# Optimization experiments

Hardware: AMD Instinct MI355X
Metric: run time of the kernel (lower is better)

The kernel has to match this reference:

```python
import jax, jax.numpy as jnp
import numpy as np

B, S, P, J = 32, 128, 2, 17
DIN, DOUT, DRNN, DHID = 2, 3, 128, 256
N = P * J
DT = 0.1   # delta_t from init
K = 4      # Euler steps, hardcoded k=int(4) in source


def setup_inputs() -> dict:
    key = jax.random.key(0)
    ks = jax.random.split(key, 12)
    g = lambda k, sh, fan: (jax.random.normal(k, sh, jnp.float32) / np.sqrt(fan)).astype(jnp.float32)
    d = {}
    d['x2d'] = jax.random.normal(ks[0], (B, S, P, J, DIN), jnp.float32)
    d['mask'] = jax.random.randint(ks[1], (B, S, P, J, 1), 0, 2).astype(jnp.int32)
    # ODE MLP: DRNN -> DHID -> DHID -> DRNN (num_hidden=2 hidden layers, tanh)
    d['ode_w0'] = g(ks[2], (DRNN, DHID), DRNN); d['ode_b0'] = jnp.zeros((DHID,), jnp.float32)
    d['ode_w1'] = g(ks[3], (DHID, DHID), DHID); d['ode_b1'] = jnp.zeros((DHID,), jnp.float32)
    d['ode_w2'] = g(ks[4], (DHID, DRNN), DHID); d['ode_b2'] = jnp.zeros((DRNN,), jnp.float32)
    # GRU cell 0: input DIN -> hidden DRNN ; GRU cell 1: input DRNN -> hidden DRNN
    d['wih0'] = g(ks[5], (DIN, 3 * DRNN), DIN);  d['whh0'] = g(ks[6], (DRNN, 3 * DRNN), DRNN)
    d['bih0'] = jnp.zeros((3 * DRNN,), jnp.float32); d['bhh0'] = jnp.zeros((3 * DRNN,), jnp.float32)
    d['wih1'] = g(ks[7], (DRNN, 3 * DRNN), DRNN); d['whh1'] = g(ks[8], (DRNN, 3 * DRNN), DRNN)
    d['bih1'] = jnp.zeros((3 * DRNN,), jnp.float32); d['bhh1'] = jnp.zeros((3 * DRNN,), jnp.float32)
    d['wout'] = g(ks[9], (DRNN, DOUT), DRNN); d['bout'] = jnp.zeros((DOUT,), jnp.float32)
    d['h0'] = 0.01 * jax.random.normal(ks[10], (1, 1, DRNN), jnp.float32)
    return d


def _ode(h, w0, b0, w1, b1, w2, b2):
    h = jnp.tanh(h @ w0 + b0)
    h = jnp.tanh(h @ w1 + b1)
    return h @ w2 + b2


def _gru(x, h, wih, whh, bih, bhh):
    gi = x @ wih + bih
    gh = h @ whh + bhh
    ir, iz, ig = jnp.split(gi, 3, axis=-1)
    hr, hz, hg = jnp.split(gh, 3, axis=-1)
    r = jax.nn.sigmoid(ir + hr)
    z = jax.nn.sigmoid(iz + hz)
    n = jnp.tanh(ig + r * hg)
    return (1.0 - z) * n + z * h


def reference(x2d, mask, ode_w0, ode_b0, ode_w1, ode_b1, ode_w2, ode_b2,
              wih0, whh0, bih0, bhh0, wih1, whh1, bih1, bhh1, wout, bout, h0):
    m = mask.astype(x2d.dtype)                      # (B,S,P,J,1)
    xs = (x2d * m).reshape(B, S, N, DIN)            # masked 2D input
    ms = m.reshape(B, S, N, 1)
    h_init = jnp.broadcast_to(h0, (B, N, DRNN))

    def step(h, inp):
        x, mm = inp                                 # (B,N,DIN), (B,N,1)
        h1 = h
        for _ in range(K):                          # 4 Euler ODE steps
            h1 = h1 + DT * _ode(h1, ode_w0, ode_b0, ode_w1, ode_b1, ode_w2, ode_b2)
        h2 = _gru(x, h1, wih0, whh0, bih0, bhh0)    # stacked GRU, both conditioned on h1
        h2 = _gru(h2, h1, wih1, whh1, bih1, bhh1)
        h_next = h1 * (1.0 - mm) + h2 * mm
        return h_next, h1

    _, hs = jax.lax.scan(step, h_init,
                         (jnp.swapaxes(xs, 0, 1), jnp.swapaxes(ms, 0, 1)))
    hs = jnp.swapaxes(hs, 0, 1)                     # (B,S,N,DRNN)
    ys = (hs @ wout + bout).reshape(B, S, P, J, DOUT)
    return ys
```

## Files before the change

kernel.cpp:

```cpp
#include <hip/hip_runtime.h>

typedef _Float16 f16x8 __attribute__((ext_vector_type(8)));
typedef float f32x4 __attribute__((ext_vector_type(4)));

constexpr int S_ = 128;
constexpr float DT_ = 0.1f;
constexpr float LS = 2048.0f;
constexpr float INV = 1.0f / 2048.0f;

#define MFMA(a, b, c) __builtin_amdgcn_mfma_f32_16x16x32_f16((a), (b), (c), 0, 0, 0)

#define OB0   0
#define OB1   256
#define OB2   512
#define OBHH0 640
#define OBIH0 1024
#define OBIH1 1408
#define OBHH1 1792
#define NBIAS 2176

__device__ __forceinline__ float fast_tanh(float x) {
    float e = __expf(2.0f * x);
    return 1.0f - 2.0f / (e + 1.0f);
}
__device__ __forceinline__ float fast_sigmoid(float x) {
    return 1.0f / (1.0f + __expf(-x));
}

__global__ void prep_hl(const float* __restrict__ src, _Float16* __restrict__ hi,
                        _Float16* __restrict__ lo, int K, int N) {
    int e = blockIdx.x * 256 + threadIdx.x;
    if (e >= K * N) return;
    int tile = e >> 9, r = e & 511;
    int lane = r >> 3, j = r & 7;
    int KT = K >> 5;
    int nt = tile / KT, kt = tile - nt * KT;
    int k = kt * 32 + ((lane >> 4) << 3) + j;
    int n = nt * 16 + (lane & 15);
    float v = src[k * N + n];
    _Float16 h = (_Float16)v;
    hi[e] = h;
    lo[e] = (_Float16)((v - (float)h) * LS);
}

__global__ __launch_bounds__(512, 2) void odernn_mfma(
    const float* __restrict__ x2d, const int* __restrict__ maskp,
    const _Float16* __restrict__ w0h, const _Float16* __restrict__ w0l,
    const _Float16* __restrict__ w1hg, const _Float16* __restrict__ w1lg,
    const _Float16* __restrict__ w2h, const _Float16* __restrict__ w2l,
    const _Float16* __restrict__ hh0h, const _Float16* __restrict__ hh0l,
    const _Float16* __restrict__ ih1h, const _Float16* __restrict__ ih1l,
    const _Float16* __restrict__ hh1h, const _Float16* __restrict__ hh1l,
    const float* __restrict__ b0, const float* __restrict__ b1,
    const float* __restrict__ b2, const float* __restrict__ bhh0,
    const float* __restrict__ bih0, const float* __restrict__ wih0,
    const float* __restrict__ bih1, const float* __restrict__ bhh1,
    const float* __restrict__ wout, const float* __restrict__ bout,
    const float* __restrict__ h0, float* __restrict__ out)
{
    __shared__ float hF[16][128];
    __shared__ _Float16 bAh[16][264], bAl[16][264];
    __shared__ _Float16 bBh[16][264], bBl[16][264];
    __shared__ _Float16 bHh[16][136], bHl[16][136];
    __shared__ float sbias[NBIAS];
    __shared__ float swi0[768];
    __shared__ float swout[384];
    __shared__ float sbout[4];
    __shared__ float sx0[16], sx1[16], smm[16];
    __shared__ int sIdx[16];

    const int tid = (int)threadIdx.x;
    const int wv = tid >> 6;
    const int l = tid & 63;
    const int lrow = l & 15;
    const int lk8 = (l >> 4) << 3;
    const int rbase = (l >> 4) << 2;

    for (int e = tid; e < 256; e += 512) { sbias[OB0 + e] = b0[e]; sbias[OB1 + e] = b1[e]; }
    for (int e = tid; e < 128; e += 512) sbias[OB2 + e] = b2[e];
    for (int e = tid; e < 384; e += 512) {
        sbias[OBHH0 + e] = bhh0[e];
        sbias[OBIH0 + e] = bih0[e];
        sbias[OBIH1 + e] = bih1[e];
        sbias[OBHH1 + e] = bhh1[e];
        swout[e] = wout[e];
    }
    for (int e = tid; e < 768; e += 512) swi0[e] = wih0[e];
    if (tid < 3) sbout[tid] = bout[tid];
    for (int e = tid; e < 2048; e += 512) hF[e >> 7][e & 127] = h0[e & 127];
    if (tid < 16) {
        int grow = (int)blockIdx.x * 16 + tid;
        int bb = grow / 34, nn = grow - bb * 34;
        sIdx[tid] = bb * (S_ * 34) + nn;
    }

    f16x8 w1rh[2][8], w1rl[2][8];
#pragma unroll
    for (int t = 0; t < 2; ++t) {
        const _Float16* ph = w1hg + (size_t)((wv + 8 * t) * 8) * 512 + l * 8;
        const _Float16* pl = w1lg + (size_t)((wv + 8 * t) * 8) * 512 + l * 8;
#pragma unroll
        for (int kt = 0; kt < 8; ++kt) {
            w1rh[t][kt] = *(const f16x8*)(ph + kt * 512);
            w1rl[t][kt] = *(const f16x8*)(pl + kt * 512);
        }
    }
    __syncthreads();

    for (int s = 0; s < S_; ++s) {
        if (tid < 16) {
            int idx = sIdx[tid] + s * 34;
            float fm = (float)maskp[idx];
            smm[tid] = fm;
            sx0[tid] = x2d[2 * idx] * fm;
            sx1[tid] = x2d[2 * idx + 1] * fm;
        }
        for (int e = tid; e < 2048; e += 512) {
            int row = e >> 7, col = e & 127;
            float v = hF[row][col];
            _Float16 hh = (_Float16)v;
            bHh[row][col] = hh;
            bHl[row][col] = (_Float16)((v - (float)hh) * LS);
        }
        __syncthreads();

        for (int it = 0; it < 4; ++it) {
            {
                const int n0 = wv << 4, n1 = (wv + 8) << 4;
                float bv0 = sbias[OB0 + n0 + lrow], bv1 = sbias[OB0 + n1 + lrow];
                f32x4 a0 = {bv0, bv0, bv0, bv0}, a1 = {bv1, bv1, bv1, bv1};
                f32x4 e0 = {0, 0, 0, 0}, e1 = {0, 0, 0, 0};
                const f16x8* B0h = (const f16x8*)(w0h + (size_t)(wv * 4) * 512) + l;
                const f16x8* B0l = (const f16x8*)(w0l + (size_t)(wv * 4) * 512) + l;
                const f16x8* B1h = (const f16x8*)(w0h + (size_t)((wv + 8) * 4) * 512) + l;
                const f16x8* B1l = (const f16x8*)(w0l + (size_t)((wv + 8) * 4) * 512) + l;
#pragma unroll
                for (int kt = 0; kt < 4; ++kt) {
                    f16x8 ah = *(const f16x8*)&bHh[lrow][kt * 32 + lk8];
                    f16x8 al = *(const f16x8*)&bHl[lrow][kt * 32 + lk8];
                    f16x8 bh0 = B0h[kt * 64], bl0 = B0l[kt * 64];
                    f16x8 bh1 = B1h[kt * 64], bl1 = B1l[kt * 64];
                    a0 = MFMA(ah, bh0, a0);
                    e0 = MFMA(ah, bl0, e0);
                    e0 = MFMA(al, bh0, e0);
                    a1 = MFMA(ah, bh1, a1);
                    e1 = MFMA(ah, bl1, e1);
                    e1 = MFMA(al, bh1, e1);
                }
#pragma unroll
                for (int r = 0; r < 4; ++r) {
                    int row = rbase + r;
                    float v0 = fast_tanh(a0[r] + e0[r] * INV);
                    float v1 = fast_tanh(a1[r] + e1[r] * INV);
                    _Float16 hh = (_Float16)v0;
                    bBh[row][n0 + lrow] = hh;
                    bBl[row][n0 + lrow] = (_Float16)((v0 - (float)hh) * LS);
                    hh = (_Float16)v1;
                    bBh[row][n1 + lrow] = hh;
                    bBl[row][n1 + lrow] = (_Float16)((v1 - (float)hh) * LS);
                }
            }
            __syncthreads();

            {
                const int n0 = wv << 4, n1 = (wv + 8) << 4;
                float bv0 = sbias[OB1 + n0 + lrow], bv1 = sbias[OB1 + n1 + lrow];
                f32x4 a0 = {bv0, bv0, bv0, bv0}, a1 = {bv1, bv1, bv1, bv1};
                f32x4 e0 = {0, 0, 0, 0}, e1 = {0, 0, 0, 0};
#pragma unroll
                for (int kt = 0; kt < 8; ++kt) {
                    f16x8 ah = *(const f16x8*)&bBh[lrow][kt * 32 + lk8];
                    f16x8 al = *(const f16x8*)&bBl[lrow][kt * 32 + lk8];
                    a0 = MFMA(ah, w1rh[0][kt], a0);
                    e0 = MFMA(ah, w1rl[0][kt], e0);
                    e0 = MFMA(al, w1rh[0][kt], e0);
                    a1 = MFMA(ah, w1rh[1][kt], a1);
                    e1 = MFMA(ah, w1rl[1][kt], e1);
                    e1 = MFMA(al, w1rh[1][kt], e1);
                }
#pragma unroll
                for (int r = 0; r < 4; ++r) {
                    int row = rbase + r;
                    float v0 = fast_tanh(a0[r] + e0[r] * INV);
                    float v1 = fast_tanh(a1[r] + e1[r] * INV);
                    _Float16 hh = (_Float16)v0;
                    bAh[row][n0 + lrow] = hh;
                    bAl[row][n0 + lrow] = (_Float16)((v0 - (float)hh) * LS);
                    hh = (_Float16)v1;
                    bAh[row][n1 + lrow] = hh;
                    bAl[row][n1 + lrow] = (_Float16)((v1 - (float)hh) * LS);
                }
            }
            __syncthreads();

            {
                const int n0 = wv << 4;
                float bv = sbias[OB2 + n0 + lrow];
                f32x4 acc = {bv, bv, bv, bv};
                f32x4 ecc = {0, 0, 0, 0};
                const f16x8* Bh = (const f16x8*)(w2h + (size_t)(wv * 8) * 512) + l;
                const f16x8* Bl = (const f16x8*)(w2l + (size_t)(wv * 8) * 512) + l;
#pragma unroll
                for (int kt = 0; kt < 8; ++kt) {
                    f16x8 ah = *(const f16x8*)&bAh[lrow][kt * 32 + lk8];
                    f16x8 al = *(const f16x8*)&bAl[lrow][kt * 32 + lk8];
                    f16x8 bh = Bh[kt * 64], bl = Bl[kt * 64];
                    acc = MFMA(ah, bh, acc);
                    ecc = MFMA(ah, bl, ecc);
                    ecc = MFMA(al, bh, ecc);
                }
#pragma unroll
                for (int r = 0; r < 4; ++r) {
                    int row = rbase + r, col = n0 + lrow;
                    float v = hF[row][col] + DT_ * (acc[r] + ecc[r] * INV);
                    hF[row][col] = v;
                    _Float16 hh = (_Float16)v;
                    bHh[row][col] = hh;
                    bHl[row][col] = (_Float16)((v - (float)hh) * LS);
                }
            }
            __syncthreads();
        }

        {
            f32x4 acc0, acc1, acc2, ecc0, ecc1, ecc2;
            {
                float v0 = sbias[OBHH0 + ((wv) << 4) + lrow];
                float v1 = sbias[OBHH0 + ((wv + 8) << 4) + lrow];
                float v2 = sbias[OBHH0 + ((wv + 16) << 4) + lrow];
                acc0 = (f32x4){v0, v0, v0, v0};
                acc1 = (f32x4){v1, v1, v1, v1};
                acc2 = (f32x4){v2, v2, v2, v2};
                ecc0 = (f32x4){0, 0, 0, 0}; ecc1 = ecc0; ecc2 = ecc0;
            }
#pragma unroll
            for (int kt = 0; kt < 4; ++kt) {
                f16x8 ah = *(const f16x8*)&bHh[lrow][kt * 32 + lk8];
                f16x8 al = *(const f16x8*)&bHl[lrow][kt * 32 + lk8];
                f16x8 bh0 = *((const f16x8*)(hh0h + (size_t)((wv) * 4 + kt) * 512) + l);
                f16x8 bl0 = *((const f16x8*)(hh0l + (size_t)((wv) * 4 + kt) * 512) + l);
                f16x8 bh1 = *((const f16x8*)(hh0h + (size_t)((wv + 8) * 4 + kt) * 512) + l);
                f16x8 bl1 = *((const f16x8*)(hh0l + (size_t)((wv + 8) * 4 + kt) * 512) + l);
                f16x8 bh2 = *((const f16x8*)(hh0h + (size_t)((wv + 16) * 4 + kt) * 512) + l);
                f16x8 bl2 = *((const f16x8*)(hh0l + (size_t)((wv + 16) * 4 + kt) * 512) + l);
                acc0 = MFMA(ah, bh0, acc0); ecc0 = MFMA(ah, bl0, ecc0); ecc0 = MFMA(al, bh0, ecc0);
                acc1 = MFMA(ah, bh1, acc1); ecc1 = MFMA(ah, bl1, ecc1); ecc1 = MFMA(al, bh1, ecc1);
                acc2 = MFMA(ah, bh2, acc2); ecc2 = MFMA(ah, bl2, ecc2); ecc2 = MFMA(al, bh2, ecc2);
            }
            {
                int yrow = wv + ((l >> 5) << 3);
                int ll = l & 31;
                int c0 = ll << 2;
                float4 hv = *(const float4*)&hF[yrow][c0];
                float p0 = hv.x * swout[c0 * 3] + hv.y * swout[(c0 + 1) * 3] +
                           hv.z * swout[(c0 + 2) * 3] + hv.w * swout[(c0 + 3) * 3];
                float p1 = hv.x * swout[c0 * 3 + 1] + hv.y * swout[(c0 + 1) * 3 + 1] +
                           hv.z * swout[(c0 + 2) * 3 + 1] + hv.w * swout[(c0 + 3) * 3 + 1];
                float p2 = hv.x * swout[c0 * 3 + 2] + hv.y * swout[(c0 + 1) * 3 + 2] +
                           hv.z * swout[(c0 + 2) * 3 + 2] + hv.w * swout[(c0 + 3) * 3 + 2];
#pragma unroll
                for (int m = 16; m >= 1; m >>= 1) {
                    p0 += __shfl_xor(p0, m, 64);
                    p1 += __shfl_xor(p1, m, 64);
                    p2 += __shfl_xor(p2, m, 64);
                }
                if (ll == 0) {
                    int idx = sIdx[yrow] + s * 34;
                    out[idx * 3 + 0] = p0 + sbout[0];
                    out[idx * 3 + 1] = p1 + sbout[1];
                    out[idx * 3 + 2] = p2 + sbout[2];
                }
            }
            {
                int col = (wv << 4) + lrow;
                float wxr0 = swi0[col], wxr1 = swi0[384 + col];
                float wxz0 = swi0[128 + col], wxz1 = swi0[384 + 128 + col];
                float wxn0 = swi0[256 + col], wxn1 = swi0[384 + 256 + col];
                float bir = sbias[OBIH0 + col], biz = sbias[OBIH0 + 128 + col], bin = sbias[OBIH0 + 256 + col];
#pragma unroll
                for (int r = 0; r < 4; ++r) {
                    int row = rbase + r;
                    float ghr = acc0[r] + ecc0[r] * INV;
                    float ghz = acc1[r] + ecc1[r] * INV;
                    float ghn = acc2[r] + ecc2[r] * INV;
                    float xa = sx0[row], xb = sx1[row];
                    float rg = fast_sigmoid(bir + xa * wxr0 + xb * wxr1 + ghr);
                    float zg = fast_sigmoid(biz + xa * wxz0 + xb * wxz1 + ghz);
                    float nn = fast_tanh(bin + xa * wxn0 + xb * wxn1 + rg * ghn);
                    float h1 = hF[row][col];
                    float h2 = (1.0f - zg) * nn + zg * h1;
                    _Float16 hh = (_Float16)h2;
                    bBh[row][col] = hh;
                    bBl[row][col] = (_Float16)((h2 - (float)hh) * LS);
                }
            }
        }
        __syncthreads();

        {
            f32x4 aI0, aI1, aI2, eI0, eI1, eI2;
            {
                float v0 = sbias[OBIH1 + ((wv) << 4) + lrow];
                float v1 = sbias[OBIH1 + ((wv + 8) << 4) + lrow];
                float v2 = sbias[OBIH1 + ((wv + 16) << 4) + lrow];
                aI0 = (f32x4){v0, v0, v0, v0};
                aI1 = (f32x4){v1, v1, v1, v1};
                aI2 = (f32x4){v2, v2, v2, v2};
                eI0 = (f32x4){0, 0, 0, 0}; eI1 = eI0; eI2 = eI0;
            }
#pragma unroll
            for (int kt = 0; kt < 4; ++kt) {
                f16x8 ah = *(const f16x8*)&bBh[lrow][kt * 32 + lk8];
                f16x8 al = *(const f16x8*)&bBl[lrow][kt * 32 + lk8];
                f16x8 bh0 = *((const f16x8*)(ih1h + (size_t)((wv) * 4 + kt) * 512) + l);
                f16x8 bl0 = *((const f16x8*)(ih1l + (size_t)((wv) * 4 + kt) * 512) + l);
                f16x8 bh1 = *((const f16x8*)(ih1h + (size_t)((wv + 8) * 4 + kt) * 512) + l);
                f16x8 bl1 = *((const f16x8*)(ih1l + (size_t)((wv + 8) * 4 + kt) * 512) + l);
                f16x8 bh2 = *((const f16x8*)(ih1h + (size_t)((wv + 16) * 4 + kt) * 512) + l);
                f16x8 bl2 = *((const f16x8*)(ih1l + (size_t)((wv + 16) * 4 + kt) * 512) + l);
                aI0 = MFMA(ah, bh0, aI0); eI0 = MFMA(ah, bl0, eI0); eI0 = MFMA(al, bh0, eI0);
                aI1 = MFMA(ah, bh1, aI1); eI1 = MFMA(ah, bl1, eI1); eI1 = MFMA(al, bh1, eI1);
                aI2 = MFMA(ah, bh2, aI2); eI2 = MFMA(ah, bl2, eI2); eI2 = MFMA(al, bh2, eI2);
            }
            f32x4 gi0 = aI0 + eI0 * INV;
            f32x4 gi1 = aI1 + eI1 * INV;
            f32x4 gi2 = aI2 + eI2 * INV;

            f32x4 aH0, aH1, aH2, eH0, eH1, eH2;
            {
                float v0 = sbias[OBHH1 + ((wv) << 4) + lrow];
                float v1 = sbias[OBHH1 + ((wv + 8) << 4) + lrow];
                float v2 = sbias[OBHH1 + ((wv + 16) << 4) + lrow];
                aH0 = (f32x4){v0, v0, v0, v0};
                aH1 = (f32x4){v1, v1, v1, v1};
                aH2 = (f32x4){v2, v2, v2, v2};
                eH0 = (f32x4){0, 0, 0, 0}; eH1 = eH0; eH2 = eH0;
            }
#pragma unroll
            for (int kt = 0; kt < 4; ++kt) {
                f16x8 ah = *(const f16x8*)&bHh[lrow][kt * 32 + lk8];
                f16x8 al = *(const f16x8*)&bHl[lrow][kt * 32 + lk8];
                f16x8 bh0 = *((const f16x8*)(hh1h + (size_t)((wv) * 4 + kt) * 512) + l);
                f16x8 bl0 = *((const f16x8*)(hh1l + (size_t)((wv) * 4 + kt) * 512) + l);
                f16x8 bh1 = *((const f16x8*)(hh1h + (size_t)((wv + 8) * 4 + kt) * 512) + l);
                f16x8 bl1 = *((const f16x8*)(hh1l + (size_t)((wv + 8) * 4 + kt) * 512) + l);
                f16x8 bh2 = *((const f16x8*)(hh1h + (size_t)((wv + 16) * 4 + kt) * 512) + l);
                f16x8 bl2 = *((const f16x8*)(hh1l + (size_t)((wv + 16) * 4 + kt) * 512) + l);
                aH0 = MFMA(ah, bh0, aH0); eH0 = MFMA(ah, bl0, eH0); eH0 = MFMA(al, bh0, eH0);
                aH1 = MFMA(ah, bh1, aH1); eH1 = MFMA(ah, bl1, eH1); eH1 = MFMA(al, bh1, eH1);
                aH2 = MFMA(ah, bh2, aH2); eH2 = MFMA(ah, bl2, eH2); eH2 = MFMA(al, bh2, eH2);
            }
#pragma unroll
            for (int r = 0; r < 4; ++r) {
                int row = rbase + r, col = (wv << 4) + lrow;
                float ghr = aH0[r] + eH0[r] * INV;
                float ghz = aH1[r] + eH1[r] * INV;
                float ghn = aH2[r] + eH2[r] * INV;
                float rg = fast_sigmoid(gi0[r] + ghr);
                float zg = fast_sigmoid(gi1[r] + ghz);
                float nn = fast_tanh(gi2[r] + rg * ghn);
                float h1 = hF[row][col];
                float h2 = (1.0f - zg) * nn + zg * h1;
                hF[row][col] = (smm[row] != 0.0f) ? h2 : h1;
            }
        }
        __syncthreads();
    }
}

extern "C" void kernel_launch(void* const* d_in, const int* in_sizes, int n_in,
                              void* d_out, int out_size, void* d_ws, size_t ws_size,
                              hipStream_t stream) {
    const float* x2d  = (const float*)d_in[0];
    const int*   mask = (const int*)d_in[1];
    const float* w0   = (const float*)d_in[2];
    const float* b0   = (const float*)d_in[3];
    const float* w1   = (const float*)d_in[4];
    const float* b1   = (const float*)d_in[5];
    const float* w2   = (const float*)d_in[6];
    const float* b2   = (const float*)d_in[7];
    const float* wih0 = (const float*)d_in[8];
    const float* whh0 = (const float*)d_in[9];
    const float* bih0 = (const float*)d_in[10];
    const float* bhh0 = (const float*)d_in[11];
    const float* wih1 = (const float*)d_in[12];
    const float* whh1 = (const float*)d_in[13];
    const float* bih1 = (const float*)d_in[14];
    const float* bhh1 = (const float*)d_in[15];
    const float* wout = (const float*)d_in[16];
    const float* bout = (const float*)d_in[17];
    const float* h0   = (const float*)d_in[18];
    float* out = (float*)d_out;

    _Float16* base = (_Float16*)d_ws;
    _Float16* pw0h  = base;
    _Float16* pw1h  = base + 32768;
    _Float16* pw2h  = base + 98304;
    _Float16* ph0h  = base + 131072;
    _Float16* pi1h  = base + 180224;
    _Float16* ph1h  = base + 229376;
    _Float16* lobase = base + 278528;
    _Float16* pw0l  = lobase;
    _Float16* pw1l  = lobase + 32768;
    _Float16* pw2l  = lobase + 98304;
    _Float16* ph0l  = lobase + 131072;
    _Float16* pi1l  = lobase + 180224;
    _Float16* ph1l  = lobase + 229376;

    hipLaunchKernelGGL(prep_hl, dim3(128), dim3(256), 0, stream, w0,   pw0h, pw0l, 128, 256);
    hipLaunchKernelGGL(prep_hl, dim3(256), dim3(256), 0, stream, w1,   pw1h, pw1l, 256, 256);
    hipLaunchKernelGGL(prep_hl, dim3(128), dim3(256), 0, stream, w2,   pw2h, pw2l, 256, 128);
    hipLaunchKernelGGL(prep_hl, dim3(192), dim3(256), 0, stream, whh0, ph0h, ph0l, 128, 384);
    hipLaunchKernelGGL(prep_hl, dim3(192), dim3(256), 0, stream, wih1, pi1h, pi1l, 128, 384);
    hipLaunchKernelGGL(prep_hl, dim3(192), dim3(256), 0, stream, whh1, ph1h, ph1l, 128, 384);

    hipLaunchKernelGGL(odernn_mfma, dim3(68), dim3(512), 0, stream,
        x2d, mask, pw0h, pw0l, pw1h, pw1l, pw2h, pw2l,
        ph0h, ph0l, pi1h, pi1l, ph1h, ph1l,
        b0, b1, b2, bhh0, bih0, wih0, bih1, bhh1, wout, bout, h0, out);
}
```

Baseline: 6.896 ms.

## Stream W1 fragments from global and fuse hidden-state split into GRU epilogue

Drops the 32 per-wave register-resident f16x8 fragments of the ODE's second-layer weight and reloads them from global/L2 each Euler step, as is already done for the other weights, to cut VGPR pressure. It also removes the per-timestep pass that splits hF into hi/lo f16 buffers and its barrier. The split is now written directly in the final GRU epilogue, with an added barrier before the epilogue so bH reads finish before the overwrite. The cost is more global weight traffic per inner iteration in exchange for lower register use and one less pass and barrier per timestep.

```diff
diff --git a/kernel.cpp b/kernel.cpp
--- a/kernel.cpp
+++ b/kernel.cpp
@@ -87,23 +87,18 @@
     }
     for (int e = tid; e < 768; e += 512) swi0[e] = wih0[e];
     if (tid < 3) sbout[tid] = bout[tid];
-    for (int e = tid; e < 2048; e += 512) hF[e >> 7][e & 127] = h0[e & 127];
+    for (int e = tid; e < 2048; e += 512) {
+        int row = e >> 7, col = e & 127;
+        float v = h0[col];
+        hF[row][col] = v;
+        _Float16 hh = (_Float16)v;
+        bHh[row][col] = hh;
+        bHl[row][col] = (_Float16)((v - (float)hh) * LS);
+    }
     if (tid < 16) {
         int grow = (int)blockIdx.x * 16 + tid;
         int bb = grow / 34, nn = grow - bb * 34;
         sIdx[tid] = bb * (S_ * 34) + nn;
-    }
-
-    f16x8 w1rh[2][8], w1rl[2][8];
-#pragma unroll
-    for (int t = 0; t < 2; ++t) {
-        const _Float16* ph = w1hg + (size_t)((wv + 8 * t) * 8) * 512 + l * 8;
-        const _Float16* pl = w1lg + (size_t)((wv + 8 * t) * 8) * 512 + l * 8;
-#pragma unroll
-        for (int kt = 0; kt < 8; ++kt) {
-            w1rh[t][kt] = *(const f16x8*)(ph + kt * 512);
-            w1rl[t][kt] = *(const f16x8*)(pl + kt * 512);
-        }
     }
     __syncthreads();
 
@@ -115,14 +110,6 @@
             sx0[tid] = x2d[2 * idx] * fm;
             sx1[tid] = x2d[2 * idx + 1] * fm;
         }
-        for (int e = tid; e < 2048; e += 512) {
-            int row = e >> 7, col = e & 127;
-            float v = hF[row][col];
-            _Float16 hh = (_Float16)v;
-            bHh[row][col] = hh;
-            bHl[row][col] = (_Float16)((v - (float)hh) * LS);
-        }
-        __syncthreads();
 
         for (int it = 0; it < 4; ++it) {
             {
@@ -167,16 +154,22 @@
                 float bv0 = sbias[OB1 + n0 + lrow], bv1 = sbias[OB1 + n1 + lrow];
                 f32x4 a0 = {bv0, bv0, bv0, bv0}, a1 = {bv1, bv1, bv1, bv1};
                 f32x4 e0 = {0, 0, 0, 0}, e1 = {0, 0, 0, 0};
+                const f16x8* B0h = (const f16x8*)(w1hg + (size_t)(wv * 8) * 512) + l;
+                const f16x8* B0l = (const f16x8*)(w1lg + (size_t)(wv * 8) * 512) + l;
+                const f16x8* B1h = (const f16x8*)(w1hg + (size_t)((wv + 8) * 8) * 512) + l;
+                const f16x8* B1l = (const f16x8*)(w1lg + (size_t)((wv + 8) * 8) * 512) + l;
 #pragma unroll
                 for (int kt = 0; kt < 8; ++kt) {
                     f16x8 ah = *(const f16x8*)&bBh[lrow][kt * 32 + lk8];
                     f16x8 al = *(const f16x8*)&bBl[lrow][kt * 32 + lk8];
-                    a0 = MFMA(ah, w1rh[0][kt], a0);
-                    e0 = MFMA(ah, w1rl[0][kt], e0);
-                    e0 = MFMA(al, w1rh[0][kt], e0);
-                    a1 = MFMA(ah, w1rh[1][kt], a1);
-                    e1 = MFMA(ah, w1rl[1][kt], e1);
-                    e1 = MFMA(al, w1rh[1][kt], e1);
+                    f16x8 bh0 = B0h[kt * 64], bl0 = B0l[kt * 64];
+                    f16x8 bh1 = B1h[kt * 64], bl1 = B1l[kt * 64];
+                    a0 = MFMA(ah, bh0, a0);
+                    e0 = MFMA(ah, bl0, e0);
+                    e0 = MFMA(al, bh0, e0);
+                    a1 = MFMA(ah, bh1, a1);
+                    e1 = MFMA(ah, bl1, e1);
+                    e1 = MFMA(al, bh1, e1);
                 }
 #pragma unroll
                 for (int r = 0; r < 4; ++r) {
@@ -350,6 +343,7 @@
                 aH1 = MFMA(ah, bh1, aH1); eH1 = MFMA(ah, bl1, eH1); eH1 = MFMA(al, bh1, eH1);
                 aH2 = MFMA(ah, bh2, aH2); eH2 = MFMA(ah, bl2, eH2); eH2 = MFMA(al, bh2, eH2);
             }
+            __syncthreads();
 #pragma unroll
             for (int r = 0; r < 4; ++r) {
                 int row = rbase + r, col = (wv << 4) + lrow;
@@ -361,7 +355,11 @@
                 float nn = fast_tanh(gi2[r] + rg * ghn);
                 float h1 = hF[row][col];
                 float h2 = (1.0f - zg) * nn + zg * h1;
-                hF[row][col] = (smm[row] != 0.0f) ? h2 : h1;
+                float v = (smm[row] != 0.0f) ? h2 : h1;
+                hF[row][col] = v;
+                _Float16 hh = (_Float16)v;
+                bHh[row][col] = hh;
+                bHl[row][col] = (_Float16)((v - (float)hh) * LS);
             }
         }
         __syncthreads();
```

Measured after the change: 6.755 ms. 2.0% less time.
